# Kernel tuning notes

Measured on AMD Instinct MI355X. Metric: run time of the kernel, lower is better.

The kernel has to match this reference:

```python
import jax, jax.numpy as jnp
import numpy as np
from jax import lax

EPS = 1e-7  # keras backend epsilon used by K.ctc_batch_cost
NEG = -1e30  # log-space 'zero'


def setup_inputs() -> dict:
    key = jax.random.key(0)
    k1, k2 = jax.random.split(key)
    B, T, C, L = 512, 512, 128, 48
    # softmax-like probabilities over classes (ctc_batch_cost expects probs)
    u = jax.random.uniform(k1, (B, T, C), dtype=jnp.float32, minval=1e-3, maxval=1.0)
    y_pred = u / jnp.sum(u, axis=-1, keepdims=True)
    # labels in [0, C-2]; blank index is C-1 (keras convention)
    y_true = jax.random.randint(k2, (B, L), 0, C - 1, dtype=jnp.int64)
    return {"y_true": y_true, "y_pred": y_pred}


def _ctc_loss(y_true, y_pred):
    # y_true: [B, L] int labels; y_pred: [B, T, C] probabilities
    B, T, C = y_pred.shape
    L = y_true.shape[1]
    S = 2 * L + 1
    blank = C - 1

    log_probs = jnp.log(y_pred + EPS)  # [B, T, C]

    # extended label sequence: blank, l1, blank, l2, ..., blank -> [B, S]
    ext = jnp.full((B, S), blank, dtype=y_true.dtype).at[:, 1::2].set(y_true)
    ext_m2 = jnp.concatenate(
        [jnp.full((B, 2), -1, dtype=ext.dtype), ext[:, :-2]], axis=1
    )
    # skip-transition allowed iff current symbol is a non-blank differing from s-2
    skip = (ext != blank) & (ext != ext_m2)  # [B, S]

    # gather per-extended-symbol log probs: [B, T, S] -> time-major [T, B, S]
    lp_ext = jnp.take_along_axis(log_probs, ext[:, None, :], axis=2)
    lp_ext = jnp.moveaxis(lp_ext, 1, 0)

    neg = jnp.asarray(NEG, log_probs.dtype)
    alpha0 = jnp.full((B, S), neg)
    alpha0 = alpha0.at[:, 0].set(lp_ext[0, :, 0]).at[:, 1].set(lp_ext[0, :, 1])

    def step(alpha, lp_t):
        a1 = alpha
        a2 = jnp.concatenate([jnp.full((B, 1), neg), alpha[:, :-1]], axis=1)
        a3 = jnp.concatenate([jnp.full((B, 2), neg), alpha[:, :-2]], axis=1)
        a3 = jnp.where(skip, a3, neg)
        new = jnp.logaddexp(jnp.logaddexp(a1, a2), a3) + lp_t
        return new, None

    alpha_T, _ = lax.scan(step, alpha0, lp_ext[1:])
    # total log-likelihood ends in last blank or last label
    loglik = jnp.logaddexp(alpha_T[:, -1], alpha_T[:, -2])
    return -loglik[:, None]  # [B, 1] like K.ctc_batch_cost


def reference(y_true, y_pred):
    return _ctc_loss(y_true, y_pred)
```

## Files before the change

kernel.cpp:

```cpp
#include <hip/hip_runtime.h>


constexpr int Bc = 512, Tc = 512, Cc = 128, Lc = 48;
constexpr float FEPS = 1e-7f;
constexpr float FNEG = -1e30f;
constexpr float LN2F = 0.69314718055994530942f;
constexpr int CDEAD = -(1 << 28);

#define DPP_WAVE_SHR1 0x138
#define DPP_WAVE_SHL1 0x130

__device__ __forceinline__ float dppf_shr1(float x) {
    return __int_as_float(__builtin_amdgcn_update_dpp(
        0, __float_as_int(x), DPP_WAVE_SHR1, 0xF, 0xF, false));
}
__device__ __forceinline__ float dppf_shl1(float x) {
    return __int_as_float(__builtin_amdgcn_update_dpp(
        0, __float_as_int(x), DPP_WAVE_SHL1, 0xF, 0xF, false));
}
__device__ __forceinline__ int dppi_shr1_self(int c) {
    return __builtin_amdgcn_update_dpp(c, c, DPP_WAVE_SHR1, 0xF, 0xF, false);
}
__device__ __forceinline__ int dppi_shl1_self(int c) {
    return __builtin_amdgcn_update_dpp(c, c, DPP_WAVE_SHL1, 0xF, 0xF, false);
}

__device__ __forceinline__ float lae2(float a, float b) {
    float m = fmaxf(a, b);
    float d = fabsf(a - b);
    return m + __log2f(1.0f + __builtin_amdgcn_exp2f(-d));
}
__device__ __forceinline__ float rd63f(float v) {
    return __uint_as_float((unsigned)
        __builtin_amdgcn_readlane(__float_as_uint(v), 63));
}

__global__ __launch_bounds__(128)
void ctc_fb_kernel(const int* __restrict__ y_true,
                   const float* __restrict__ y_pred,
                   float* __restrict__ out) {
    const int b = blockIdx.x;
    const int lane = threadIdx.x & 63;
    const int wave = threadIdx.x >> 6;

    const float* yb = y_pred + (size_t)b * Tc * Cc;

    const int lab = (lane < Lc) ? y_true[b * Lc + lane] : (Cc - 1);
    const int labm1 = __builtin_amdgcn_ds_bpermute(((lane + 63) & 63) << 2, lab);
    const bool skip  = (lab != (Cc - 1)) && (lab != labm1);
    const bool validhi = (lane < Lc);
    const bool lane0 = (lane == 0);

    __shared__ float sblo[64], sbhi[64];
    __shared__ int sbc[64];

    float lo = 0.0f, hi = 0.0f;
    int c = CDEAD;

    auto renorm = [&]() {
        float mx = fmaxf(lo, hi);
        int e = (int)((__float_as_uint(mx) >> 23) & 0xFF) - 127;
        e = (mx > 0.0f) ? e : 0;
        lo = ldexpf(lo, -e);
        hi = ldexpf(hi, -e);
        c += e;
    };

    float praw[16], pbf[16], phf[16];
    auto batch = [&]() {
        #pragma unroll
        for (int j = 0; j < 16; ++j) {
            pbf[j] = rd63f(praw[j]) + FEPS;
            phf[j] = validhi ? (praw[j] + FEPS) : 0.0f;
        }
    };

    if (wave == 0) {
        auto step = [&](int j) {
            float sh  = dppf_shr1(hi);
            int   cm1 = dppi_shr1_self(c);
            bool  own_dead = (lo == 0.0f) && (hi == 0.0f);
            int   m  = own_dead ? cm1 : ((c > cm1) ? c : cm1);
            float lov = ldexpf(lo, c - m);
            float hiv = ldexpf(hi, c - m);
            float shv = ldexpf(sh, cm1 - m);
            float a3  = skip ? shv : 0.0f;
            lo = (lov + shv) * pbf[j];
            hi = (hiv + lov + a3) * phf[j];
            c = m;
        };
        #pragma unroll
        for (int j = 0; j < 16; ++j) praw[j] = yb[j * Cc + lab];
        {
            batch();
            const float* ybn = yb + (size_t)16 * Cc + lab;
            #pragma unroll
            for (int j = 0; j < 16; ++j) praw[j] = ybn[(size_t)j * Cc];
            lo = lane0 ? pbf[0] : 0.0f;
            hi = lane0 ? phf[0] : 0.0f;
            c  = lane0 ? 0 : CDEAD;
            #pragma unroll
            for (int j = 1; j < 16; ++j) {
                step(j);
                if (j == 7 || j == 15) renorm();
            }
        }
        #pragma unroll 1
        for (int g = 1; g < 16; ++g) {
            batch();
            if (g < 15) {
                const float* ybn = yb + (size_t)((g + 1) * 16) * Cc + lab;
                #pragma unroll
                for (int j = 0; j < 16; ++j) praw[j] = ybn[(size_t)j * Cc];
            }
            #pragma unroll
            for (int j = 0; j < 16; ++j) {
                step(j);
                if (j == 7 || j == 15) renorm();
            }
        }
    } else {
        auto step = [&](int j) {
            float qlo = lo * pbf[j];
            float qhi = hi * phf[j];
            float u   = qlo + (skip ? qhi : 0.0f);
            float un  = dppf_shl1(u);
            int   cp1 = dppi_shl1_self(c);
            bool  own_dead = (qlo == 0.0f) && (qhi == 0.0f);
            int   m  = own_dead ? cp1 : ((c > cp1) ? c : cp1);
            lo = ldexpf(qlo + qhi, c - m);
            hi = ldexpf(qhi, c - m) + ldexpf(un, cp1 - m);
            c = m;
        };
        lo = (lane == 48) ? 1.0f : 0.0f;
        hi = (lane == 47) ? 1.0f : 0.0f;
        c  = (lane == 47 || lane == 48) ? 0 : CDEAD;
        #pragma unroll
        for (int j = 0; j < 16; ++j) praw[j] = yb[(size_t)(511 - j) * Cc + lab];
        #pragma unroll 1
        for (int g = 0; g < 16; ++g) {
            batch();
            if (g < 15) {
                const float* ybn = yb + lab;
                const int t0 = 511 - (g + 1) * 16;
                #pragma unroll
                for (int j = 0; j < 16; ++j) praw[j] = ybn[(size_t)(t0 - j) * Cc];
            }
            #pragma unroll
            for (int j = 0; j < 16; ++j) {
                step(j);
                if (j == 7 || j == 15) renorm();
            }
        }
        sblo[lane] = lo;
        sbhi[lane] = hi;
        sbc[lane]  = c;
    }

    __syncthreads();

    if (wave == 0) {
        float blo = sblo[lane], bhi = sbhi[lane];
        float ctot = (float)(c + sbc[lane]);
        float plo = lo * blo;
        float phi = hi * bhi;
        float yl = (plo > 0.0f) ? (__log2f(plo) + ctot) : FNEG;
        float yh = (phi > 0.0f) ? (__log2f(phi) + ctot) : FNEG;
        float v = lae2(yl, yh);
        #pragma unroll
        for (int mk = 1; mk < 64; mk <<= 1)
            v = lae2(v, __shfl_xor(v, mk, 64));
        if (lane0) out[b] = -(v * LN2F);
    }
}

extern "C" void kernel_launch(void* const* d_in, const int* in_sizes, int n_in,
                              void* d_out, int out_size, void* d_ws, size_t ws_size,
                              hipStream_t stream) {
    const int* y_true = (const int*)d_in[0];
    const float* y_pred = (const float*)d_in[1];
    float* out = (float*)d_out;
    hipLaunchKernelGGL(ctc_fb_kernel, dim3(Bc), dim3(128), 0, stream,
                       y_true, y_pred, out);
}
```

Before: 29.82 us.

## Split loads into producer waves feeding an LDS ring buffer via global_load_lds

Adds two producer waves per block that issue global_load_lds gathers of the per-label probabilities into an 8-deep LDS ring, one ring per direction. They signal readiness through workgroup-scope atomic counters. The forward and backward recurrence waves consume from the ring instead of doing their own register-prefetched global loads, which is meant to hide memory latency better and free VGPRs. In exchange it doubles the block size, adds spin-wait polling with s_sleep, and relies on hand-counted vmcnt waits, which is fragile.

Result: slower. 32.94 us (+10.5%).

```diff
diff --git a/kernel.cpp b/kernel.cpp
--- a/kernel.cpp
+++ b/kernel.cpp
@@ -6,9 +6,12 @@
 constexpr float FNEG = -1e30f;
 constexpr float LN2F = 0.69314718055994530942f;
 constexpr int CDEAD = -(1 << 28);
+constexpr int NG = 16;
+constexpr int RD = 8;
 
 #define DPP_WAVE_SHR1 0x138
 #define DPP_WAVE_SHL1 0x130
+#define WG __HIP_MEMORY_SCOPE_WORKGROUP
 
 __device__ __forceinline__ float dppf_shr1(float x) {
     return __int_as_float(__builtin_amdgcn_update_dpp(
@@ -24,7 +27,6 @@
 __device__ __forceinline__ int dppi_shl1_self(int c) {
     return __builtin_amdgcn_update_dpp(c, c, DPP_WAVE_SHL1, 0xF, 0xF, false);
 }
-
 __device__ __forceinline__ float lae2(float a, float b) {
     float m = fmaxf(a, b);
     float d = fabsf(a - b);
@@ -35,143 +37,171 @@
         __builtin_amdgcn_readlane(__float_as_uint(v), 63));
 }
 
-__global__ __launch_bounds__(128)
-void ctc_fb_kernel(const int* __restrict__ y_true,
+typedef const __attribute__((address_space(1))) void* gptr_t;
+typedef __attribute__((address_space(3))) void* lptr_t;
+__device__ __forceinline__ void gload(const float* g, float* l) {
+    __builtin_amdgcn_global_load_lds((gptr_t)g, (lptr_t)l, 4, 0, 0);
+}
+
+__global__ __launch_bounds__(256)
+void ctc_pc_kernel(const int* __restrict__ y_true,
                    const float* __restrict__ y_pred,
                    float* __restrict__ out) {
     const int b = blockIdx.x;
-    const int lane = threadIdx.x & 63;
-    const int wave = threadIdx.x >> 6;
-
-    const float* yb = y_pred + (size_t)b * Tc * Cc;
-
-    const int lab = (lane < Lc) ? y_true[b * Lc + lane] : (Cc - 1);
-    const int labm1 = __builtin_amdgcn_ds_bpermute(((lane + 63) & 63) << 2, lab);
-    const bool skip  = (lab != (Cc - 1)) && (lab != labm1);
-    const bool validhi = (lane < Lc);
-    const bool lane0 = (lane == 0);
-
+    const int tid = threadIdx.x;
+    const int lane = tid & 63;
+    const int wid = tid >> 6;
+
+    __shared__ float ring[2][RD][16][64];
+    __shared__ int ready[2], done[2];
     __shared__ float sblo[64], sbhi[64];
     __shared__ int sbc[64];
 
-    float lo = 0.0f, hi = 0.0f;
-    int c = CDEAD;
-
-    auto renorm = [&]() {
-        float mx = fmaxf(lo, hi);
-        int e = (int)((__float_as_uint(mx) >> 23) & 0xFF) - 127;
-        e = (mx > 0.0f) ? e : 0;
-        lo = ldexpf(lo, -e);
-        hi = ldexpf(hi, -e);
-        c += e;
-    };
-
-    float praw[16], pbf[16], phf[16];
-    auto batch = [&]() {
-        #pragma unroll
-        for (int j = 0; j < 16; ++j) {
-            pbf[j] = rd63f(praw[j]) + FEPS;
-            phf[j] = validhi ? (praw[j] + FEPS) : 0.0f;
-        }
-    };
-
-    if (wave == 0) {
-        auto step = [&](int j) {
-            float sh  = dppf_shr1(hi);
-            int   cm1 = dppi_shr1_self(c);
-            bool  own_dead = (lo == 0.0f) && (hi == 0.0f);
-            int   m  = own_dead ? cm1 : ((c > cm1) ? c : cm1);
-            float lov = ldexpf(lo, c - m);
-            float hiv = ldexpf(hi, c - m);
-            float shv = ldexpf(sh, cm1 - m);
-            float a3  = skip ? shv : 0.0f;
-            lo = (lov + shv) * pbf[j];
-            hi = (hiv + lov + a3) * phf[j];
-            c = m;
+    const float* yb = y_pred + (size_t)b * Tc * Cc;
+    const int lab = (lane < Lc) ? y_true[b * Lc + lane] : (Cc - 1);
+
+    if (tid == 0) { ready[0] = ready[1] = 0; done[0] = done[1] = 0; }
+    __syncthreads();
+
+    if (wid >= 2) {
+        const int d = wid - 2;
+        #pragma unroll 1
+        for (int g = 0; g < NG; ++g) {
+            if (g >= RD) {
+                while (__hip_atomic_load(&done[d], __ATOMIC_RELAXED, WG) < g - (RD - 1))
+                    __builtin_amdgcn_s_sleep(1);
+            }
+            float* lb = &ring[d][g & (RD - 1)][0][0];
+            const int t0 = d ? (511 - g * 16) : (g * 16);
+            #pragma unroll
+            for (int j = 0; j < 16; ++j) {
+                const int t = d ? (t0 - j) : (t0 + j);
+                gload(yb + (size_t)t * Cc + lab, lb + j * 64);
+            }
+            if (g >= 3) {
+                asm volatile("s_waitcnt vmcnt(48)" ::: "memory");
+                __builtin_amdgcn_sched_barrier(0);
+                if (lane == 0)
+                    __hip_atomic_store(&ready[d], g - 2, __ATOMIC_RELAXED, WG);
+                __builtin_amdgcn_sched_barrier(0);
+            }
+        }
+        asm volatile("s_waitcnt vmcnt(32)" ::: "memory");
+        __builtin_amdgcn_sched_barrier(0);
+        if (lane == 0) __hip_atomic_store(&ready[d], NG - 2, __ATOMIC_RELAXED, WG);
+        asm volatile("s_waitcnt vmcnt(16)" ::: "memory");
+        __builtin_amdgcn_sched_barrier(0);
+        if (lane == 0) __hip_atomic_store(&ready[d], NG - 1, __ATOMIC_RELAXED, WG);
+        asm volatile("s_waitcnt vmcnt(0)" ::: "memory");
+        __builtin_amdgcn_sched_barrier(0);
+        if (lane == 0) __hip_atomic_store(&ready[d], NG, __ATOMIC_RELAXED, WG);
+    } else {
+        const int dir = wid;
+        const int labm1 = __builtin_amdgcn_ds_bpermute(((lane + 63) & 63) << 2, lab);
+        const bool skip = (lab != (Cc - 1)) && (lab != labm1);
+        const bool validhi = (lane < Lc);
+        const bool lane0 = (lane == 0);
+
+        float lo = 0.0f, hi = 0.0f;
+        int c = CDEAD;
+
+        auto renorm = [&]() {
+            float mx = fmaxf(lo, hi);
+            int e = (int)((__float_as_uint(mx) >> 23) & 0xFF) - 127;
+            e = (mx > 0.0f) ? e : 0;
+            lo = ldexpf(lo, -e);
+            hi = ldexpf(hi, -e);
+            c += e;
         };
-        #pragma unroll
-        for (int j = 0; j < 16; ++j) praw[j] = yb[j * Cc + lab];
-        {
-            batch();
-            const float* ybn = yb + (size_t)16 * Cc + lab;
-            #pragma unroll
-            for (int j = 0; j < 16; ++j) praw[j] = ybn[(size_t)j * Cc];
-            lo = lane0 ? pbf[0] : 0.0f;
-            hi = lane0 ? phf[0] : 0.0f;
-            c  = lane0 ? 0 : CDEAD;
-            #pragma unroll
-            for (int j = 1; j < 16; ++j) {
-                step(j);
-                if (j == 7 || j == 15) renorm();
-            }
-        }
+
+        float praw[16], pbf[16], phf[16];
+
+        if (dir == 1) {
+            lo = (lane == 48) ? 1.0f : 0.0f;
+            hi = (lane == 47) ? 1.0f : 0.0f;
+            c  = (lane == 47 || lane == 48) ? 0 : CDEAD;
+        }
+
         #pragma unroll 1
-        for (int g = 1; g < 16; ++g) {
-            batch();
-            if (g < 15) {
-                const float* ybn = yb + (size_t)((g + 1) * 16) * Cc + lab;
+        for (int g = 0; g < NG; ++g) {
+            while (__hip_atomic_load(&ready[dir], __ATOMIC_RELAXED, WG) < g + 1)
+                __builtin_amdgcn_s_sleep(1);
+            __builtin_amdgcn_sched_barrier(0);
+            #pragma unroll
+            for (int j = 0; j < 16; ++j) praw[j] = ring[dir][g & (RD - 1)][j][lane];
+            #pragma unroll
+            for (int j = 0; j < 16; ++j) {
+                pbf[j] = rd63f(praw[j]) + FEPS;
+                phf[j] = validhi ? (praw[j] + FEPS) : 0.0f;
+            }
+            if (dir == 0) {
+                int j0 = 0;
+                if (g == 0) {
+                    lo = lane0 ? pbf[0] : 0.0f;
+                    hi = lane0 ? phf[0] : 0.0f;
+                    c  = lane0 ? 0 : CDEAD;
+                    j0 = 1;
+                }
                 #pragma unroll
-                for (int j = 0; j < 16; ++j) praw[j] = ybn[(size_t)j * Cc];
-            }
-            #pragma unroll
-            for (int j = 0; j < 16; ++j) {
-                step(j);
-                if (j == 7 || j == 15) renorm();
-            }
-        }
-    } else {
-        auto step = [&](int j) {
-            float qlo = lo * pbf[j];
-            float qhi = hi * phf[j];
-            float u   = qlo + (skip ? qhi : 0.0f);
-            float un  = dppf_shl1(u);
-            int   cp1 = dppi_shl1_self(c);
-            bool  own_dead = (qlo == 0.0f) && (qhi == 0.0f);
-            int   m  = own_dead ? cp1 : ((c > cp1) ? c : cp1);
-            lo = ldexpf(qlo + qhi, c - m);
-            hi = ldexpf(qhi, c - m) + ldexpf(un, cp1 - m);
-            c = m;
-        };
-        lo = (lane == 48) ? 1.0f : 0.0f;
-        hi = (lane == 47) ? 1.0f : 0.0f;
-        c  = (lane == 47 || lane == 48) ? 0 : CDEAD;
-        #pragma unroll
-        for (int j = 0; j < 16; ++j) praw[j] = yb[(size_t)(511 - j) * Cc + lab];
-        #pragma unroll 1
-        for (int g = 0; g < 16; ++g) {
-            batch();
-            if (g < 15) {
-                const float* ybn = yb + lab;
-                const int t0 = 511 - (g + 1) * 16;
+                for (int j = 0; j < 16; ++j) {
+                    if (j < j0) continue;
+                    float sh  = dppf_shr1(hi);
+                    int   cm1 = dppi_shr1_self(c);
+                    bool  own_dead = (lo == 0.0f) && (hi == 0.0f);
+                    int   m  = own_dead ? cm1 : ((c > cm1) ? c : cm1);
+                    float lov = ldexpf(lo, c - m);
+                    float hiv = ldexpf(hi, c - m);
+                    float shv = ldexpf(sh, cm1 - m);
+                    float a3  = skip ? shv : 0.0f;
+                    lo = (lov + shv) * pbf[j];
+                    hi = (hiv + lov + a3) * phf[j];
+                    c = m;
+                    if (j == 7 || j == 15) renorm();
+                }
+            } else {
                 #pragma unroll
-                for (int j = 0; j < 16; ++j) praw[j] = ybn[(size_t)(t0 - j) * Cc];
-            }
-            #pragma unroll
-            for (int j = 0; j < 16; ++j) {
-                step(j);
-                if (j == 7 || j == 15) renorm();
-            }
-        }
-        sblo[lane] = lo;
-        sbhi[lane] = hi;
-        sbc[lane]  = c;
+                for (int j = 0; j < 16; ++j) {
+                    float qlo = lo * pbf[j];
+                    float qhi = hi * phf[j];
+                    float u   = qlo + (skip ? qhi : 0.0f);
+                    float un  = dppf_shl1(u);
+                    int   cp1 = dppi_shl1_self(c);
+                    bool  own_dead = (qlo == 0.0f) && (qhi == 0.0f);
+                    int   m  = own_dead ? cp1 : ((c > cp1) ? c : cp1);
+                    lo = ldexpf(qlo + qhi, c - m);
+                    hi = ldexpf(qhi, c - m) + ldexpf(un, cp1 - m);
+                    c = m;
+                    if (j == 7 || j == 15) renorm();
+                }
+            }
+            __builtin_amdgcn_sched_barrier(0);
+            if (lane == 0)
+                __hip_atomic_store(&done[dir], g + 1, __ATOMIC_RELAXED, WG);
+        }
+
+        if (dir == 1) {
+            sblo[lane] = lo;
+            sbhi[lane] = hi;
+            sbc[lane]  = c;
+        } else {
+        }
+        __syncthreads();
+        if (dir == 0) {
+            float blo = sblo[lane], bhi = sbhi[lane];
+            float ctot = (float)(c + sbc[lane]);
+            float plo = lo * blo;
+            float phi = hi * bhi;
+            float yl = (plo > 0.0f) ? (__log2f(plo) + ctot) : FNEG;
+            float yh = (phi > 0.0f) ? (__log2f(phi) + ctot) : FNEG;
+            float v = lae2(yl, yh);
+            #pragma unroll
+            for (int mk = 1; mk < 64; mk <<= 1)
+                v = lae2(v, __shfl_xor(v, mk, 64));
+            if (lane0) out[b] = -(v * LN2F);
+        }
+        return;
     }
-
     __syncthreads();
-
-    if (wave == 0) {
-        float blo = sblo[lane], bhi = sbhi[lane];
-        float ctot = (float)(c + sbc[lane]);
-        float plo = lo * blo;
-        float phi = hi * bhi;
-        float yl = (plo > 0.0f) ? (__log2f(plo) + ctot) : FNEG;
-        float yh = (phi > 0.0f) ? (__log2f(phi) + ctot) : FNEG;
-        float v = lae2(yl, yh);
-        #pragma unroll
-        for (int mk = 1; mk < 64; mk <<= 1)
-            v = lae2(v, __shfl_xor(v, mk, 64));
-        if (lane0) out[b] = -(v * LN2F);
-    }
 }
 
 extern "C" void kernel_launch(void* const* d_in, const int* in_sizes, int n_in,
@@ -180,6 +210,6 @@
     const int* y_true = (const int*)d_in[0];
     const float* y_pred = (const float*)d_in[1];
     float* out = (float*)d_out;
-    hipLaunchKernelGGL(ctc_fb_kernel, dim3(Bc), dim3(128), 0, stream,
+    hipLaunchKernelGGL(ctc_pc_kernel, dim3(Bc), dim3(256), 0, stream,
                        y_true, y_pred, out);
 }
```

## Process two batch items per block to interleave independent recurrence chains

Applied to the files above, without the earlier changes.

Each block now handles two batch elements, with every wave running two independent forward (or backward) recurrences interleaved step by step. The aim is to hide the serial DPP/ldexp dependency latency of one chain behind the other (ILP), and to halve the block count from 512 to 256. The cost is higher register pressure (doubled prefetch arrays) and fewer blocks, which may leave CUs idle on a 256-CU device.

Result: slower. 36.46 us (+22.3%).

```diff
diff --git a/kernel.cpp b/kernel.cpp
--- a/kernel.cpp
+++ b/kernel.cpp
@@ -24,7 +24,6 @@
 __device__ __forceinline__ int dppi_shl1_self(int c) {
     return __builtin_amdgcn_update_dpp(c, c, DPP_WAVE_SHL1, 0xF, 0xF, false);
 }
-
 __device__ __forceinline__ float lae2(float a, float b) {
     float m = fmaxf(a, b);
     float d = fabsf(a - b);
@@ -36,141 +35,201 @@
 }
 
 __global__ __launch_bounds__(128)
-void ctc_fb_kernel(const int* __restrict__ y_true,
-                   const float* __restrict__ y_pred,
-                   float* __restrict__ out) {
-    const int b = blockIdx.x;
+void ctc_fb2_kernel(const int* __restrict__ y_true,
+                    const float* __restrict__ y_pred,
+                    float* __restrict__ out) {
+    const int bA = blockIdx.x * 2;
+    const int bB = bA + 1;
     const int lane = threadIdx.x & 63;
     const int wave = threadIdx.x >> 6;
 
-    const float* yb = y_pred + (size_t)b * Tc * Cc;
-
-    const int lab = (lane < Lc) ? y_true[b * Lc + lane] : (Cc - 1);
-    const int labm1 = __builtin_amdgcn_ds_bpermute(((lane + 63) & 63) << 2, lab);
-    const bool skip  = (lab != (Cc - 1)) && (lab != labm1);
+    const float* ybA = y_pred + (size_t)bA * Tc * Cc;
+    const float* ybB = y_pred + (size_t)bB * Tc * Cc;
+
+    const int labA = (lane < Lc) ? y_true[bA * Lc + lane] : (Cc - 1);
+    const int labB = (lane < Lc) ? y_true[bB * Lc + lane] : (Cc - 1);
+    const int pa = ((lane + 63) & 63) << 2;
+    const int labm1A = __builtin_amdgcn_ds_bpermute(pa, labA);
+    const int labm1B = __builtin_amdgcn_ds_bpermute(pa, labB);
+    const bool skipA = (labA != (Cc - 1)) && (labA != labm1A);
+    const bool skipB = (labB != (Cc - 1)) && (labB != labm1B);
     const bool validhi = (lane < Lc);
     const bool lane0 = (lane == 0);
 
-    __shared__ float sblo[64], sbhi[64];
-    __shared__ int sbc[64];
-
-    float lo = 0.0f, hi = 0.0f;
-    int c = CDEAD;
-
-    auto renorm = [&]() {
-        float mx = fmaxf(lo, hi);
-        int e = (int)((__float_as_uint(mx) >> 23) & 0xFF) - 127;
-        e = (mx > 0.0f) ? e : 0;
-        lo = ldexpf(lo, -e);
-        hi = ldexpf(hi, -e);
-        c += e;
+    __shared__ float sblo[2][64], sbhi[2][64];
+    __shared__ int sbc[2][64];
+
+    float loA = 0.0f, hiA = 0.0f, loB = 0.0f, hiB = 0.0f;
+    int cA = CDEAD, cB = CDEAD;
+
+    auto renorm2 = [&]() {
+        float mxA = fmaxf(loA, hiA);
+        float mxB = fmaxf(loB, hiB);
+        int eA = (int)((__float_as_uint(mxA) >> 23) & 0xFF) - 127;
+        int eB = (int)((__float_as_uint(mxB) >> 23) & 0xFF) - 127;
+        eA = (mxA > 0.0f) ? eA : 0;
+        eB = (mxB > 0.0f) ? eB : 0;
+        loA = ldexpf(loA, -eA); hiA = ldexpf(hiA, -eA);
+        loB = ldexpf(loB, -eB); hiB = ldexpf(hiB, -eB);
+        cA += eA; cB += eB;
     };
 
-    float praw[16], pbf[16], phf[16];
-    auto batch = [&]() {
+    float prA[16], prB[16], pbA[16], phA[16], pbB[16], phB[16];
+    auto batch2 = [&]() {
         #pragma unroll
         for (int j = 0; j < 16; ++j) {
-            pbf[j] = rd63f(praw[j]) + FEPS;
-            phf[j] = validhi ? (praw[j] + FEPS) : 0.0f;
+            pbA[j] = rd63f(prA[j]) + FEPS;
+            phA[j] = validhi ? (prA[j] + FEPS) : 0.0f;
+            pbB[j] = rd63f(prB[j]) + FEPS;
+            phB[j] = validhi ? (prB[j] + FEPS) : 0.0f;
         }
     };
 
     if (wave == 0) {
-        auto step = [&](int j) {
-            float sh  = dppf_shr1(hi);
-            int   cm1 = dppi_shr1_self(c);
-            bool  own_dead = (lo == 0.0f) && (hi == 0.0f);
-            int   m  = own_dead ? cm1 : ((c > cm1) ? c : cm1);
-            float lov = ldexpf(lo, c - m);
-            float hiv = ldexpf(hi, c - m);
-            float shv = ldexpf(sh, cm1 - m);
-            float a3  = skip ? shv : 0.0f;
-            lo = (lov + shv) * pbf[j];
-            hi = (hiv + lov + a3) * phf[j];
-            c = m;
+        auto step2 = [&](int j) {
+            float shA = dppf_shr1(hiA);
+            float shB = dppf_shr1(hiB);
+            int cm1A = dppi_shr1_self(cA);
+            int cm1B = dppi_shr1_self(cB);
+            bool dA = (loA == 0.0f) && (hiA == 0.0f);
+            bool dB = (loB == 0.0f) && (hiB == 0.0f);
+            int mA = dA ? cm1A : ((cA > cm1A) ? cA : cm1A);
+            int mB = dB ? cm1B : ((cB > cm1B) ? cB : cm1B);
+            float lovA = ldexpf(loA, cA - mA), lovB = ldexpf(loB, cB - mB);
+            float hivA = ldexpf(hiA, cA - mA), hivB = ldexpf(hiB, cB - mB);
+            float shvA = ldexpf(shA, cm1A - mA), shvB = ldexpf(shB, cm1B - mB);
+            float a3A = skipA ? shvA : 0.0f, a3B = skipB ? shvB : 0.0f;
+            loA = (lovA + shvA) * pbA[j];
+            hiA = (hivA + lovA + a3A) * phA[j];
+            loB = (lovB + shvB) * pbB[j];
+            hiB = (hivB + lovB + a3B) * phB[j];
+            cA = mA; cB = mB;
         };
         #pragma unroll
-        for (int j = 0; j < 16; ++j) praw[j] = yb[j * Cc + lab];
+        for (int j = 0; j < 16; ++j) {
+            prA[j] = ybA[j * Cc + labA];
+            prB[j] = ybB[j * Cc + labB];
+        }
         {
-            batch();
-            const float* ybn = yb + (size_t)16 * Cc + lab;
-            #pragma unroll
-            for (int j = 0; j < 16; ++j) praw[j] = ybn[(size_t)j * Cc];
-            lo = lane0 ? pbf[0] : 0.0f;
-            hi = lane0 ? phf[0] : 0.0f;
-            c  = lane0 ? 0 : CDEAD;
+            batch2();
+            const float* ybnA = ybA + (size_t)16 * Cc + labA;
+            const float* ybnB = ybB + (size_t)16 * Cc + labB;
+            #pragma unroll
+            for (int j = 0; j < 16; ++j) {
+                prA[j] = ybnA[(size_t)j * Cc];
+                prB[j] = ybnB[(size_t)j * Cc];
+            }
+            loA = lane0 ? pbA[0] : 0.0f;
+            hiA = lane0 ? phA[0] : 0.0f;
+            loB = lane0 ? pbB[0] : 0.0f;
+            hiB = lane0 ? phB[0] : 0.0f;
+            cA = lane0 ? 0 : CDEAD;
+            cB = lane0 ? 0 : CDEAD;
             #pragma unroll
             for (int j = 1; j < 16; ++j) {
-                step(j);
-                if (j == 7 || j == 15) renorm();
+                step2(j);
+                if (j == 7 || j == 15) renorm2();
             }
         }
         #pragma unroll 1
         for (int g = 1; g < 16; ++g) {
-            batch();
+            batch2();
             if (g < 15) {
-                const float* ybn = yb + (size_t)((g + 1) * 16) * Cc + lab;
+                const float* ybnA = ybA + (size_t)((g + 1) * 16) * Cc + labA;
+                const float* ybnB = ybB + (size_t)((g + 1) * 16) * Cc + labB;
                 #pragma unroll
-                for (int j = 0; j < 16; ++j) praw[j] = ybn[(size_t)j * Cc];
+                for (int j = 0; j < 16; ++j) {
+                    prA[j] = ybnA[(size_t)j * Cc];
+                    prB[j] = ybnB[(size_t)j * Cc];
+                }
             }
             #pragma unroll
             for (int j = 0; j < 16; ++j) {
-                step(j);
-                if (j == 7 || j == 15) renorm();
+                step2(j);
+                if (j == 7 || j == 15) renorm2();
             }
         }
     } else {
-        auto step = [&](int j) {
-            float qlo = lo * pbf[j];
-            float qhi = hi * phf[j];
-            float u   = qlo + (skip ? qhi : 0.0f);
-            float un  = dppf_shl1(u);
-            int   cp1 = dppi_shl1_self(c);
-            bool  own_dead = (qlo == 0.0f) && (qhi == 0.0f);
-            int   m  = own_dead ? cp1 : ((c > cp1) ? c : cp1);
-            lo = ldexpf(qlo + qhi, c - m);
-            hi = ldexpf(qhi, c - m) + ldexpf(un, cp1 - m);
-            c = m;
+        auto step2 = [&](int j) {
+            float qloA = loA * pbA[j];
+            float qhiA = hiA * phA[j];
+            float qloB = loB * pbB[j];
+            float qhiB = hiB * phB[j];
+            float uA = qloA + (skipA ? qhiA : 0.0f);
+            float uB = qloB + (skipB ? qhiB : 0.0f);
+            float unA = dppf_shl1(uA);
+            float unB = dppf_shl1(uB);
+            int cp1A = dppi_shl1_self(cA);
+            int cp1B = dppi_shl1_self(cB);
+            bool dA = (qloA == 0.0f) && (qhiA == 0.0f);
+            bool dB = (qloB == 0.0f) && (qhiB == 0.0f);
+            int mA = dA ? cp1A : ((cA > cp1A) ? cA : cp1A);
+            int mB = dB ? cp1B : ((cB > cp1B) ? cB : cp1B);
+            loA = ldexpf(qloA + qhiA, cA - mA);
+            hiA = ldexpf(qhiA, cA - mA) + ldexpf(unA, cp1A - mA);
+            loB = ldexpf(qloB + qhiB, cB - mB);
+            hiB = ldexpf(qhiB, cB - mB) + ldexpf(unB, cp1B - mB);
+            cA = mA; cB = mB;
         };
-        lo = (lane == 48) ? 1.0f : 0.0f;
-        hi = (lane == 47) ? 1.0f : 0.0f;
-        c  = (lane == 47 || lane == 48) ? 0 : CDEAD;
+        loA = (lane == 48) ? 1.0f : 0.0f;
+        hiA = (lane == 47) ? 1.0f : 0.0f;
+        loB = (lane == 48) ? 1.0f : 0.0f;
+        hiB = (lane == 47) ? 1.0f : 0.0f;
+        cA = (lane == 47 || lane == 48) ? 0 : CDEAD;
+        cB = cA;
         #pragma unroll
-        for (int j = 0; j < 16; ++j) praw[j] = yb[(size_t)(511 - j) * Cc + lab];
+        for (int j = 0; j < 16; ++j) {
+            prA[j] = ybA[(size_t)(511 - j) * Cc + labA];
+            prB[j] = ybB[(size_t)(511 - j) * Cc + labB];
+        }
         #pragma unroll 1
         for (int g = 0; g < 16; ++g) {
-            batch();
+            batch2();
             if (g < 15) {
-                const float* ybn = yb + lab;
                 const int t0 = 511 - (g + 1) * 16;
                 #pragma unroll
-                for (int j = 0; j < 16; ++j) praw[j] = ybn[(size_t)(t0 - j) * Cc];
+                for (int j = 0; j < 16; ++j) {
+                    prA[j] = ybA[(size_t)(t0 - j) * Cc + labA];
+                    prB[j] = ybB[(size_t)(t0 - j) * Cc + labB];
+                }
             }
             #pragma unroll
             for (int j = 0; j < 16; ++j) {
-                step(j);
-                if (j == 7 || j == 15) renorm();
-            }
-        }
-        sblo[lane] = lo;
-        sbhi[lane] = hi;
-        sbc[lane]  = c;
+                step2(j);
+                if (j == 7 || j == 15) renorm2();
+            }
+        }
+        sblo[0][lane] = loA; sbhi[0][lane] = hiA; sbc[0][lane] = cA;
+        sblo[1][lane] = loB; sbhi[1][lane] = hiB; sbc[1][lane] = cB;
     }
 
     __syncthreads();
 
     if (wave == 0) {
-        float blo = sblo[lane], bhi = sbhi[lane];
-        float ctot = (float)(c + sbc[lane]);
-        float plo = lo * blo;
-        float phi = hi * bhi;
-        float yl = (plo > 0.0f) ? (__log2f(plo) + ctot) : FNEG;
-        float yh = (phi > 0.0f) ? (__log2f(phi) + ctot) : FNEG;
-        float v = lae2(yl, yh);
-        #pragma unroll
-        for (int mk = 1; mk < 64; mk <<= 1)
-            v = lae2(v, __shfl_xor(v, mk, 64));
-        if (lane0) out[b] = -(v * LN2F);
+        {
+            float ctot = (float)(cA + sbc[0][lane]);
+            float plo = loA * sblo[0][lane];
+            float phi = hiA * sbhi[0][lane];
+            float yl = (plo > 0.0f) ? (__log2f(plo) + ctot) : FNEG;
+            float yh = (phi > 0.0f) ? (__log2f(phi) + ctot) : FNEG;
+            float v = lae2(yl, yh);
+            #pragma unroll
+            for (int mk = 1; mk < 64; mk <<= 1)
+                v = lae2(v, __shfl_xor(v, mk, 64));
+            if (lane0) out[bA] = -(v * LN2F);
+        }
+        {
+            float ctot = (float)(cB + sbc[1][lane]);
+            float plo = loB * sblo[1][lane];
+            float phi = hiB * sbhi[1][lane];
+            float yl = (plo > 0.0f) ? (__log2f(plo) + ctot) : FNEG;
+            float yh = (phi > 0.0f) ? (__log2f(phi) + ctot) : FNEG;
+            float v = lae2(yl, yh);
+            #pragma unroll
+            for (int mk = 1; mk < 64; mk <<= 1)
+                v = lae2(v, __shfl_xor(v, mk, 64));
+            if (lane0) out[bB] = -(v * LN2F);
+        }
     }
 }
 
@@ -180,6 +239,6 @@
     const int* y_true = (const int*)d_in[0];
     const float* y_pred = (const float*)d_in[1];
     float* out = (float*)d_out;
-    hipLaunchKernelGGL(ctc_fb_kernel, dim3(Bc), dim3(128), 0, stream,
+    hipLaunchKernelGGL(ctc_fb2_kernel, dim3(Bc / 2), dim3(128), 0, stream,
                        y_true, y_pred, out);
 }
```
